# Kernel tuning notes

Hardware: AMD Instinct MI355X
Metric: run time of the kernel (lower is better)

The kernel has to match this reference:

```python
import jax, jax.numpy as jnp
from jax import lax
import numpy as np

B, T, I, H, OUT = 4096, 168, 4, 64, 12


def setup_inputs() -> dict:
    key = jax.random.key(0)
    ks = jax.random.split(key, 14)
    s = 0.05
    return {
        "x": jax.random.normal(ks[0], (B, T, I), dtype=jnp.float32),
        # LSTM layer 0 (PyTorch gate order: i, f, g, o)
        "Wih0": jax.random.normal(ks[1], (4 * H, I), dtype=jnp.float32) * s,
        "Whh0": jax.random.normal(ks[2], (4 * H, H), dtype=jnp.float32) * s,
        "bih0": jax.random.normal(ks[3], (4 * H,), dtype=jnp.float32) * s,
        "bhh0": jax.random.normal(ks[4], (4 * H,), dtype=jnp.float32) * s,
        # LSTM layer 1
        "Wih1": jax.random.normal(ks[5], (4 * H, H), dtype=jnp.float32) * s,
        "Whh1": jax.random.normal(ks[6], (4 * H, H), dtype=jnp.float32) * s,
        "bih1": jax.random.normal(ks[7], (4 * H,), dtype=jnp.float32) * s,
        "bhh1": jax.random.normal(ks[8], (4 * H,), dtype=jnp.float32) * s,
        # FC head: Linear(64,64) -> ReLU -> Linear(64,12)
        "W1": jax.random.normal(ks[9], (64, H), dtype=jnp.float32) * s,
        "b1": jax.random.normal(ks[10], (64,), dtype=jnp.float32) * s,
        "W2": jax.random.normal(ks[11], (OUT, 64), dtype=jnp.float32) * s,
        "b2": jax.random.normal(ks[12], (OUT,), dtype=jnp.float32) * s,
    }


def _lstm_layer(x, Wih, Whh, bih, bhh):
    # x: [B, T, in]; returns hidden sequence [B, T, H]
    Bsz = x.shape[0]
    Hd = Whh.shape[1]
    # Precompute input contribution for all timesteps: [B, T, 4H]
    xg = jnp.einsum('bti,gi->btg', x, Wih) + bih + bhh

    def step(carry, xg_t):
        h, c = carry
        g = xg_t + h @ Whh.T  # [B, 4H]
        i, f, gg, o = jnp.split(g, 4, axis=-1)
        i = jax.nn.sigmoid(i)
        f = jax.nn.sigmoid(f)
        gg = jnp.tanh(gg)
        o = jax.nn.sigmoid(o)
        c = f * c + i * gg
        h = o * jnp.tanh(c)
        return (h, c), h

    h0 = jnp.zeros((Bsz, Hd), x.dtype)
    (_, _), hs = lax.scan(step, (h0, h0), jnp.swapaxes(xg, 0, 1))  # hs: [T, B, H]
    return jnp.swapaxes(hs, 0, 1)


def reference(x, Wih0, Whh0, bih0, bhh0, Wih1, Whh1, bih1, bhh1, W1, b1, W2, b2):
    # Eval-mode forward: dropout layers are identity.
    h1 = _lstm_layer(x, Wih0, Whh0, bih0, bhh0)   # [B, T, H]
    h2 = _lstm_layer(h1, Wih1, Whh1, bih1, bhh1)  # [B, T, H]
    last = h2[:, -1, :]                            # [B, H]
    z = jax.nn.relu(last @ W1.T + b1)              # [B, 64]
    out = z @ W2.T + b2                            # [B, 12]
    return out.reshape(-1, 3, 4)
```

## Files before the change

### kernel.cpp

```cpp
#include <hip/hip_runtime.h>


typedef _Float16 h8 __attribute__((ext_vector_type(8)));
typedef _Float16 h4 __attribute__((ext_vector_type(4)));
typedef float f4 __attribute__((ext_vector_type(4)));

#define ROWB 208
#define HBUF (16 * ROWB)
#define XTAB_OFF 0
#define XTAB_BYTES (169 * 256)
#define H0_OFF XTAB_BYTES
#define H1_OFF (H0_OFF + 2 * HBUF)
#define SMEM_TOTAL (H1_OFF + 2 * HBUF)

#define K1F 1.4426950408889634f
#define K2F 2.8853900817779268f

__device__ __forceinline__ float exp2_(float x) {
#if __has_builtin(__builtin_amdgcn_exp2f)
  return __builtin_amdgcn_exp2f(x);
#else
  float r; asm("v_exp_f32 %0, %1" : "=v"(r) : "v"(x)); return r;
#endif
}
__device__ __forceinline__ float rcp_(float x) {
#if __has_builtin(__builtin_amdgcn_rcpf)
  return __builtin_amdgcn_rcpf(x);
#else
  float r; asm("v_rcp_f32 %0, %1" : "=v"(r) : "v"(x)); return r;
#endif
}

__device__ __forceinline__ f4 mfma16(h8 a, h8 b, f4 c) {
  return __builtin_amdgcn_mfma_f32_16x16x32_f16(a, b, c, 0, 0, 0);
}

__device__ __forceinline__ h8 load_w8s(const float* __restrict__ p, float sc) {
  h8 r;
#pragma unroll
  for (int j = 0; j < 8; j++) r[j] = (_Float16)(p[j] * sc);
  return r;
}

__device__ __forceinline__ void lstm_act(f4 a, float& c, float& h) {
  float Ei = exp2_(-a[0]);
  float Ef = exp2_(-a[1]);
  float Eg = exp2_(a[2]);
  float Eo = exp2_(-a[3]);
  float A = 1.f + Ei, B = 1.f + Ef, C = 1.f + Eg, D = 1.f + Eo;
  float AB = A * B, CD = C * D, BD = B * D;
  float R  = rcp_(AB * CD);
  float fv = (A * CD) * R;
  float ig = (BD * (Eg - 1.f)) * R;
  float ov = (AB * C) * R;
  c = fv * c + ig;
  float r2 = rcp_(exp2_(c * K2F) + 1.f);
  h = ov * (1.f - 2.f * r2);
}

extern "C" __global__ void __launch_bounds__(1024, 4)
weather_lstm_mfma5(const float* __restrict__ x,
                   const float* __restrict__ Wih0, const float* __restrict__ Whh0,
                   const float* __restrict__ bih0, const float* __restrict__ bhh0,
                   const float* __restrict__ Wih1, const float* __restrict__ Whh1,
                   const float* __restrict__ bih1, const float* __restrict__ bhh1,
                   const float* __restrict__ W1, const float* __restrict__ b1,
                   const float* __restrict__ W2, const float* __restrict__ b2,
                   float* __restrict__ out)
{
  __shared__ __align__(16) unsigned char smem[SMEM_TOTAL];
  const int tid  = threadIdx.x;
  const int lane = tid & 63;
  const int w    = tid >> 6;
  const int col  = lane & 15;
  const int quad = lane >> 4;
  const int sB   = blockIdx.x * 16;

  const int g_  = col & 3;
  const int ul_ = col >> 2;
  const float asc = (g_ == 2) ? K2F : K1F;
  const int r = g_ * 64 + w * 4 + ul_;

  h8 a0[3], a1i[2], a1h[2];
#pragma unroll
  for (int f = 0; f < 2; f++) {
    a0[f]  = load_w8s(Whh0 + r * 64 + f * 32 + quad * 8, asc);
    a1i[f] = load_w8s(Wih1 + r * 64 + f * 32 + quad * 8, asc);
    a1h[f] = load_w8s(Whh1 + r * 64 + f * 32 + quad * 8, asc);
  }
  {
    h8 xw = {};
    if (quad == 0) {
#pragma unroll
      for (int j = 0; j < 4; j++) xw[j] = (_Float16)(Wih0[r * 4 + j] * asc);
    }
    a0[2] = xw;
  }

  f4 bias0v, bias1v;
#pragma unroll
  for (int reg = 0; reg < 4; reg++) {
    const int rr = reg * 64 + w * 4 + quad;
    const float bs = (reg == 2) ? K2F : K1F;
    bias0v[reg] = (bih0[rr] + bhh0[rr]) * bs;
    bias1v[reg] = (bih1[rr] + bhh1[rr]) * bs;
  }

  for (int idx = tid; idx < SMEM_TOTAL / 4; idx += 1024) ((int*)smem)[idx] = 0;
  __syncthreads();
  for (int idx = tid; idx < 16 * 168; idx += 1024) {
    const int c_ = idx / 168, t_ = idx - c_ * 168;
    f4 xv = *(const f4*)(x + ((size_t)(sB + c_) * 168 + t_) * 4);
    h4 xh;
#pragma unroll
    for (int j = 0; j < 4; j++) xh[j] = (_Float16)xv[j];
    *(h4*)(smem + XTAB_OFF + t_ * 256 + c_ * 16) = xh;
  }
  __syncthreads();

  float c0 = 0.f, c1 = 0.f, hl = 0.f;
  const int bo = col * ROWB + quad * 16;
  const int wo = col * ROWB + (w * 4 + quad) * 2;
  const unsigned char* xp = smem + XTAB_OFF + col * 16;

  for (int k = 0; k <= 168; k++) {
    const int kb = k & 1, kbn = kb ^ 1;
    const unsigned char* h0r = smem + H0_OFF + kbn * HBUF;
    unsigned char*       h0w = smem + H0_OFF + kb  * HBUF;
    const unsigned char* h1r = smem + H1_OFF + kb  * HBUF;
    unsigned char*       h1w = smem + H1_OFF + kbn * HBUF;

    h8 b0  = *(const h8*)(h0r + bo);
    h8 b1v = *(const h8*)(h0r + bo + 64);
    h8 bx  = *(const h8*)(xp + k * 256);
    h8 q0  = *(const h8*)(h1r + bo);
    h8 q1  = *(const h8*)(h1r + bo + 64);

    f4 A0 = mfma16(a0[0], b0, bias0v);
    f4 C0 = mfma16(a1i[0], b0, bias1v);
    A0 = mfma16(a0[1], b1v, A0);
    C0 = mfma16(a1i[1], b1v, C0);
    A0 = mfma16(a0[2], bx, A0);
    C0 = mfma16(a1h[0], q0, C0);
    C0 = mfma16(a1h[1], q1, C0);

    if (k < 168) {
      float h0o;
      lstm_act(A0, c0, h0o);
      *(_Float16*)(h0w + wo) = (_Float16)h0o;
    }
    if (k > 0) {
      lstm_act(C0, c1, hl);
      *(_Float16*)(h1w + wo) = (_Float16)hl;
    }
    __syncthreads();
  }

  float* fh = (float*)smem;
  fh[col * 64 + (w * 4 + quad)] = hl;
  __syncthreads();

  {
    const int u = tid & 63, grp = tid >> 6;
    float za = b1[u];
    const float* w1r = W1 + u * 64;
    const float* f0 = fh + grp * 64;
    for (int j = 0; j < 64; j++) za += w1r[j] * f0[j];
    float* zl = (float*)(smem + 4096);
    zl[grp * 64 + u] = fmaxf(za, 0.f);
  }
  __syncthreads();

  if (tid < 192) {
    const float* zl = (const float*)(smem + 4096);
    const int s = tid / 12, o = tid - s * 12;
    float a = b2[o];
    for (int j = 0; j < 64; j++) a += W2[o * 64 + j] * zl[s * 64 + j];
    out[(sB + s) * 12 + o] = a;
  }
}

extern "C" void kernel_launch(void* const* d_in, const int* in_sizes, int n_in,
                              void* d_out, int out_size, void* d_ws, size_t ws_size,
                              hipStream_t stream) {
  (void)in_sizes; (void)n_in; (void)d_ws; (void)ws_size; (void)out_size;
  const float* x    = (const float*)d_in[0];
  const float* Wih0 = (const float*)d_in[1];
  const float* Whh0 = (const float*)d_in[2];
  const float* bih0 = (const float*)d_in[3];
  const float* bhh0 = (const float*)d_in[4];
  const float* Wih1 = (const float*)d_in[5];
  const float* Whh1 = (const float*)d_in[6];
  const float* bih1 = (const float*)d_in[7];
  const float* bhh1 = (const float*)d_in[8];
  const float* W1   = (const float*)d_in[9];
  const float* b1   = (const float*)d_in[10];
  const float* W2   = (const float*)d_in[11];
  const float* b2   = (const float*)d_in[12];

  weather_lstm_mfma5<<<dim3(256), dim3(1024), 0, stream>>>(
      x, Wih0, Whh0, bih0, bhh0, Wih1, Whh1, bih1, bhh1, W1, b1, W2, b2,
      (float*)d_out);
}
```

Before: 225.5 us.

## Shrink block to four waves, each computing four MFMA tiles of hidden units

Each block drops from 16 waves to 4, and each wave now owns 16 hidden units through four interleaved MFMA tiles per gate group. Weights and biases for all four tiles stay in registers, and stores become packed half2 writes. The aim is to cut per-step barrier cost across waves and give each wave independent MFMA chains to hide latency. In exchange, register pressure and per-wave serial activation work both rise, and fewer waves per CU are left to hide latency.

```diff
diff --git a/kernel.cpp b/kernel.cpp
--- a/kernel.cpp
+++ b/kernel.cpp
@@ -40,6 +40,12 @@
 #pragma unroll
   for (int j = 0; j < 8; j++) r[j] = (_Float16)(p[j] * sc);
   return r;
+}
+
+__device__ __forceinline__ unsigned packh2(float a, float b) {
+  unsigned lo = (unsigned)__builtin_bit_cast(unsigned short, (_Float16)a);
+  unsigned hi = (unsigned)__builtin_bit_cast(unsigned short, (_Float16)b);
+  return lo | (hi << 16);
 }
 
 __device__ __forceinline__ void lstm_act(f4 a, float& c, float& h) {
@@ -58,8 +64,8 @@
   h = ov * (1.f - 2.f * r2);
 }
 
-extern "C" __global__ void __launch_bounds__(1024, 4)
-weather_lstm_mfma5(const float* __restrict__ x,
+extern "C" __global__ void __launch_bounds__(256, 1)
+weather_lstm_mfma6(const float* __restrict__ x,
                    const float* __restrict__ Wih0, const float* __restrict__ Whh0,
                    const float* __restrict__ bih0, const float* __restrict__ bhh0,
                    const float* __restrict__ Wih1, const float* __restrict__ Whh1,
@@ -75,40 +81,46 @@
   const int col  = lane & 15;
   const int quad = lane >> 4;
   const int sB   = blockIdx.x * 16;
+  const int ub   = w * 16;
 
   const int g_  = col & 3;
   const int ul_ = col >> 2;
   const float asc = (g_ == 2) ? K2F : K1F;
-  const int r = g_ * 64 + w * 4 + ul_;
-
-  h8 a0[3], a1i[2], a1h[2];
-#pragma unroll
-  for (int f = 0; f < 2; f++) {
-    a0[f]  = load_w8s(Whh0 + r * 64 + f * 32 + quad * 8, asc);
-    a1i[f] = load_w8s(Wih1 + r * 64 + f * 32 + quad * 8, asc);
-    a1h[f] = load_w8s(Whh1 + r * 64 + f * 32 + quad * 8, asc);
-  }
-  {
+
+  h8 a0[4][3], a1i[4][2], a1h[4][2];
+#pragma unroll
+  for (int T = 0; T < 4; T++) {
+    const int unit = ub + (T >> 1) * 8 + 2 * ul_ + (T & 1);
+    const int r = g_ * 64 + unit;
+#pragma unroll
+    for (int f = 0; f < 2; f++) {
+      a0[T][f]  = load_w8s(Whh0 + r * 64 + f * 32 + quad * 8, asc);
+      a1i[T][f] = load_w8s(Wih1 + r * 64 + f * 32 + quad * 8, asc);
+      a1h[T][f] = load_w8s(Whh1 + r * 64 + f * 32 + quad * 8, asc);
+    }
     h8 xw = {};
     if (quad == 0) {
 #pragma unroll
       for (int j = 0; j < 4; j++) xw[j] = (_Float16)(Wih0[r * 4 + j] * asc);
     }
-    a0[2] = xw;
-  }
-
-  f4 bias0v, bias1v;
-#pragma unroll
-  for (int reg = 0; reg < 4; reg++) {
-    const int rr = reg * 64 + w * 4 + quad;
-    const float bs = (reg == 2) ? K2F : K1F;
-    bias0v[reg] = (bih0[rr] + bhh0[rr]) * bs;
-    bias1v[reg] = (bih1[rr] + bhh1[rr]) * bs;
-  }
-
-  for (int idx = tid; idx < SMEM_TOTAL / 4; idx += 1024) ((int*)smem)[idx] = 0;
-  __syncthreads();
-  for (int idx = tid; idx < 16 * 168; idx += 1024) {
+    a0[T][2] = xw;
+  }
+
+  f4 bias0v[4], bias1v[4];
+#pragma unroll
+  for (int T = 0; T < 4; T++) {
+#pragma unroll
+    for (int reg = 0; reg < 4; reg++) {
+      const int rr = reg * 64 + ub + (T >> 1) * 8 + 2 * quad + (T & 1);
+      const float bs = (reg == 2) ? K2F : K1F;
+      bias0v[T][reg] = (bih0[rr] + bhh0[rr]) * bs;
+      bias1v[T][reg] = (bih1[rr] + bhh1[rr]) * bs;
+    }
+  }
+
+  for (int idx = tid; idx < SMEM_TOTAL / 4; idx += 256) ((int*)smem)[idx] = 0;
+  __syncthreads();
+  for (int idx = tid; idx < 16 * 168; idx += 256) {
     const int c_ = idx / 168, t_ = idx - c_ * 168;
     f4 xv = *(const f4*)(x + ((size_t)(sB + c_) * 168 + t_) * 4);
     h4 xh;
@@ -118,9 +130,11 @@
   }
   __syncthreads();
 
-  float c0 = 0.f, c1 = 0.f, hl = 0.f;
-  const int bo = col * ROWB + quad * 16;
-  const int wo = col * ROWB + (w * 4 + quad) * 2;
+  float c0[4] = {0.f, 0.f, 0.f, 0.f}, c1[4] = {0.f, 0.f, 0.f, 0.f};
+  float hl[4] = {0.f, 0.f, 0.f, 0.f};
+  const int bo  = col * ROWB + quad * 16;
+  const int wo0 = col * ROWB + (ub + 2 * quad) * 2;
+  const int wo1 = wo0 + 16;
   const unsigned char* xp = smem + XTAB_OFF + col * 16;
 
   for (int k = 0; k <= 168; k++) {
@@ -136,38 +150,59 @@
     h8 q0  = *(const h8*)(h1r + bo);
     h8 q1  = *(const h8*)(h1r + bo + 64);
 
-    f4 A0 = mfma16(a0[0], b0, bias0v);
-    f4 C0 = mfma16(a1i[0], b0, bias1v);
-    A0 = mfma16(a0[1], b1v, A0);
-    C0 = mfma16(a1i[1], b1v, C0);
-    A0 = mfma16(a0[2], bx, A0);
-    C0 = mfma16(a1h[0], q0, C0);
-    C0 = mfma16(a1h[1], q1, C0);
+    f4 A[4], C[4];
+#pragma unroll
+    for (int T = 0; T < 4; T++) A[T] = mfma16(a0[T][0], b0, bias0v[T]);
+#pragma unroll
+    for (int T = 0; T < 4; T++) C[T] = mfma16(a1i[T][0], b0, bias1v[T]);
+#pragma unroll
+    for (int T = 0; T < 4; T++) A[T] = mfma16(a0[T][1], b1v, A[T]);
+#pragma unroll
+    for (int T = 0; T < 4; T++) C[T] = mfma16(a1i[T][1], b1v, C[T]);
+#pragma unroll
+    for (int T = 0; T < 4; T++) A[T] = mfma16(a0[T][2], bx, A[T]);
+#pragma unroll
+    for (int T = 0; T < 4; T++) C[T] = mfma16(a1h[T][0], q0, C[T]);
+#pragma unroll
+    for (int T = 0; T < 4; T++) C[T] = mfma16(a1h[T][1], q1, C[T]);
 
     if (k < 168) {
-      float h0o;
-      lstm_act(A0, c0, h0o);
-      *(_Float16*)(h0w + wo) = (_Float16)h0o;
+      float h0o[4];
+#pragma unroll
+      for (int T = 0; T < 4; T++) lstm_act(A[T], c0[T], h0o[T]);
+      *(unsigned*)(h0w + wo0) = packh2(h0o[0], h0o[1]);
+      *(unsigned*)(h0w + wo1) = packh2(h0o[2], h0o[3]);
     }
     if (k > 0) {
-      lstm_act(C0, c1, hl);
-      *(_Float16*)(h1w + wo) = (_Float16)hl;
+#pragma unroll
+      for (int T = 0; T < 4; T++) lstm_act(C[T], c1[T], hl[T]);
+      *(unsigned*)(h1w + wo0) = packh2(hl[0], hl[1]);
+      *(unsigned*)(h1w + wo1) = packh2(hl[2], hl[3]);
     }
     __syncthreads();
   }
 
   float* fh = (float*)smem;
-  fh[col * 64 + (w * 4 + quad)] = hl;
+#pragma unroll
+  for (int T = 0; T < 4; T++)
+    fh[col * 64 + (ub + (T >> 1) * 8 + 2 * quad + (T & 1))] = hl[T];
   __syncthreads();
 
   {
     const int u = tid & 63, grp = tid >> 6;
-    float za = b1[u];
+    float za[4];
+#pragma unroll
+    for (int i = 0; i < 4; i++) za[i] = b1[u];
     const float* w1r = W1 + u * 64;
-    const float* f0 = fh + grp * 64;
-    for (int j = 0; j < 64; j++) za += w1r[j] * f0[j];
+    for (int j = 0; j < 64; j++) {
+      float wv = w1r[j];
+#pragma unroll
+      for (int i = 0; i < 4; i++) za[i] += wv * fh[(grp * 4 + i) * 64 + j];
+    }
     float* zl = (float*)(smem + 4096);
-    zl[grp * 64 + u] = fmaxf(za, 0.f);
+#pragma unroll
+    for (int i = 0; i < 4; i++)
+      zl[(grp * 4 + i) * 64 + u] = fmaxf(za[i], 0.f);
   }
   __syncthreads();
 
@@ -198,7 +233,7 @@
   const float* W2   = (const float*)d_in[11];
   const float* b2   = (const float*)d_in[12];
 
-  weather_lstm_mfma5<<<dim3(256), dim3(1024), 0, stream>>>(
+  weather_lstm_mfma6<<<dim3(256), dim3(256), 0, stream>>>(
       x, Wih0, Whh0, bih0, bhh0, Wih1, Whh1, bih1, bhh1, W1, b1, W2, b2,
       (float*)d_out);
 }
```

New measurement: 234.7 us. 1.04x slower.
